# Optimization experiments

Measured on AMD Instinct MI355X. Metric: run time of the kernel, lower is better.

The kernel has to match this reference:

```python
import jax, jax.numpy as jnp
import numpy as np

FRAC_BITS = 16            # fixed-point fractional bits (MPC fixedpoint precision)
SCALE = float(1 << FRAC_BITS)

def fxp(v):
    """Emulate dup_with_precision: round value to the fixed-point grid with
    FRAC_BITS fractional bits. Straight-through (identity) gradient, matching
    the MPC backward pass which propagates gradients through truncation."""
    return v + jax.lax.stop_gradient(jnp.round(v * SCALE) / SCALE - v)


def setup_inputs() -> dict:
    key = jax.random.key(0)
    kx, kw = jax.random.split(key)
    in_dim, out_dim, batch = 4096, 4096, 2048
    x = jax.random.normal(kx, (batch, in_dim), dtype=jnp.float32)
    # Dense_Local init: w ~ N(0, 1/sqrt(in_dim+1)), b = zeros
    w = jax.random.normal(kw, (in_dim, out_dim), dtype=jnp.float32) / np.sqrt(in_dim + 1)
    b = jnp.zeros((out_dim,), dtype=jnp.float32)
    return {"x": x, "w": w, "b": b}


def reference(x, w, b):
    # quantize operands to the fixed-point grid (values live on the grid in MPC)
    xq = fxp(x)
    wq = fxp(w)
    # y = x @ w, then dup_with_precision(x.fixedpoint): truncate product back
    y = fxp(jnp.matmul(xq, wq))           # [batch, out_dim]
    # + bias
    y = y + fxp(b)
    # secure ReLU: s = drelu_local(y) (sign bit), y = relu(y, s) = y * s
    s = y >= 0
    y = jnp.where(s, y, jnp.zeros((), dtype=y.dtype))
    # final dup_with_precision(new_fixedpoint=x.fixedpoint)
    return fxp(y)
```

## Files before the change

### kernel.cpp

```cpp
#include <hip/hip_runtime.h>
#include <hip/hip_bf16.h>
#include <stdint.h>

#define M_DIM 2048
#define N_DIM 4096
#define K_DIM 4096

#define NT 64

typedef short short8 __attribute__((ext_vector_type(8)));
typedef float f32x4 __attribute__((ext_vector_type(4)));

typedef __attribute__((address_space(1))) unsigned int gu32;
typedef __attribute__((address_space(3))) unsigned int lu32;

__device__ static inline unsigned short f32_to_bf16(float f) {
  union { float f; unsigned int u; } v; v.f = f;
  unsigned int u = v.u;
  u += 0x7FFFu + ((u >> 16) & 1u);
  return (unsigned short)(u >> 16);
}

__global__ void cvt_x_kernel(const float* __restrict__ in, unsigned short* __restrict__ out) {
  size_t i = ((size_t)blockIdx.x * blockDim.x + threadIdx.x) * 8;
  f32x4 a = *(const f32x4*)(in + i);
  f32x4 b = *(const f32x4*)(in + i + 4);
  short8 o;
  o[0] = (short)f32_to_bf16(a[0]); o[1] = (short)f32_to_bf16(a[1]);
  o[2] = (short)f32_to_bf16(a[2]); o[3] = (short)f32_to_bf16(a[3]);
  o[4] = (short)f32_to_bf16(b[0]); o[5] = (short)f32_to_bf16(b[1]);
  o[6] = (short)f32_to_bf16(b[2]); o[7] = (short)f32_to_bf16(b[3]);
  *(short8*)(out + i) = o;
}

__global__ void transpose_cvt_w_kernel(const float* __restrict__ w, unsigned short* __restrict__ wt) {
  __shared__ unsigned short tile[64][64 + 8];
  int bn = blockIdx.x * 64;
  int bk = blockIdx.y * 64;
  int t = threadIdx.x;
  int c4 = (t & 15) * 4;
  int r0 = t >> 4;
#pragma unroll
  for (int p = 0; p < 4; ++p) {
    int r = r0 + p * 16;
    f32x4 v = *(const f32x4*)(w + (size_t)(bk + r) * N_DIM + bn + c4);
    tile[c4 + 0][r] = f32_to_bf16(v[0]);
    tile[c4 + 1][r] = f32_to_bf16(v[1]);
    tile[c4 + 2][r] = f32_to_bf16(v[2]);
    tile[c4 + 3][r] = f32_to_bf16(v[3]);
  }
  __syncthreads();
  int orow = t >> 2;
  int oc = (t & 3) * 16;
  short8 lo, hi;
#pragma unroll
  for (int j = 0; j < 8; ++j) {
    lo[j] = (short)tile[orow][oc + j];
    hi[j] = (short)tile[orow][oc + 8 + j];
  }
  unsigned short* op = wt + (size_t)(bn + orow) * K_DIM + bk + oc;
  *(short8*)(op) = lo;
  *(short8*)(op + 8) = hi;
}


__global__ __launch_bounds__(512) void gemm8_kernel(
    const unsigned short* __restrict__ A, const unsigned short* __restrict__ Bt,
    const float* __restrict__ bias, float* __restrict__ C) {
  __shared__ unsigned short sm16[3 * 24576];
  char* smem = (char*)&sm16[0];

  const int tid = threadIdx.x;
  const int lane = tid & 63;
  const int w = tid >> 6;
  const int wm = w >> 2, wn = w & 3;

  const int id = blockIdx.x;
  const int x = id & 7, j = id >> 3;
  const int by = ((x >> 2) << 3) + (j >> 2);
  const int bx = ((x & 3) << 2) + (j & 3);
  const int r0 = by * 128, c0 = bx * 256;

  const int l8 = lane >> 3, l7 = lane & 7;
  const int chunkE = ((l7 ^ (l8 & 7)) << 3);
  const unsigned short* Ag = A + (size_t)(r0 + w * 16 + l8) * K_DIM + chunkE;
  const unsigned short* Bg = Bt + (size_t)(c0 + w * 32 + l8) * K_DIM + chunkE;
  const int aL0 = w * 2048;
  const int bL0 = 16384 + w * 4096;

#define GL(gp, ldsoff) __builtin_amdgcn_global_load_lds((gu32*)(gp), (lu32*)(smem + (ldsoff)), 16, 0, 0)
#define STAGE_ALL(t, sb)                                               \
  do {                                                                 \
    GL(Ag + (size_t)(t) * 64, (sb) + aL0);                             \
    GL(Ag + (size_t)(t) * 64 + 8 * (size_t)K_DIM, (sb) + aL0 + 1024);  \
    GL(Bg + (size_t)(t) * 64, (sb) + bL0);                             \
    GL(Bg + (size_t)(t) * 64 + 8 * (size_t)K_DIM, (sb) + bL0 + 1024);  \
    GL(Bg + (size_t)(t) * 64 + 16 * (size_t)K_DIM, (sb) + bL0 + 2048); \
    GL(Bg + (size_t)(t) * 64 + 24 * (size_t)K_DIM, (sb) + bL0 + 3072); \
  } while (0)

  const int l15 = lane & 15, hi = lane >> 4;
  const int aR = (wm * 64 + l15) * 64;
  const int bR = 8192 + (wn * 64 + l15) * 64;
  const int slot0 = ((hi ^ l7) << 3);
  const int slot1 = (((4 + hi) ^ l7) << 3);

  f32x4 acc[4][4] = {};

  STAGE_ALL(0, 0);
  STAGE_ALL(1, 49152);

  int cs = 0;
  for (int t = 0; t < NT; ++t) {
    const int sE = cs * 24576;
    const int stB = (cs == 0 ? 2 : cs - 1) * 49152;
    const bool doStage = (t + 2) < NT;

    if (t < NT - 1) asm volatile("s_waitcnt vmcnt(6) lgkmcnt(0)" ::: "memory");
    else            asm volatile("s_waitcnt vmcnt(0) lgkmcnt(0)" ::: "memory");
    __builtin_amdgcn_sched_barrier(0);
    asm volatile("s_barrier" ::: "memory");

    short8 a0[4], b0[4], a1[4], b1[4];
#pragma unroll
    for (int m = 0; m < 4; ++m) a0[m] = *(const short8*)(sm16 + sE + aR + m * 1024 + slot0);
#pragma unroll
    for (int n = 0; n < 4; ++n) b0[n] = *(const short8*)(sm16 + sE + bR + n * 1024 + slot0);
    if (doStage) STAGE_ALL(t + 2, stB);
#pragma unroll
    for (int m = 0; m < 4; ++m) a1[m] = *(const short8*)(sm16 + sE + aR + m * 1024 + slot1);
#pragma unroll
    for (int n = 0; n < 4; ++n) b1[n] = *(const short8*)(sm16 + sE + bR + n * 1024 + slot1);

    __builtin_amdgcn_s_setprio(1);
#pragma unroll
    for (int m = 0; m < 4; ++m)
#pragma unroll
      for (int n = 0; n < 4; ++n)
        acc[m][n] = __builtin_amdgcn_mfma_f32_16x16x32_bf16(a0[m], b0[n], acc[m][n], 0, 0, 0);
#pragma unroll
    for (int m = 0; m < 4; ++m)
#pragma unroll
      for (int n = 0; n < 4; ++n)
        acc[m][n] = __builtin_amdgcn_mfma_f32_16x16x32_bf16(a1[m], b1[n], acc[m][n], 0, 0, 0);
    __builtin_amdgcn_s_setprio(0);

    cs = (cs == 2) ? 0 : cs + 1;
  }

  const float S = 65536.0f, IS = 1.0f / 65536.0f;
  const int lr = hi * 4;
#pragma unroll
  for (int n = 0; n < 4; ++n) {
    int gcol = c0 + wn * 64 + n * 16 + l15;
    float bq = rintf(bias[gcol] * S) * IS;
#pragma unroll
    for (int m = 0; m < 4; ++m) {
      int grow = r0 + wm * 64 + m * 16 + lr;
      float* outp = C + (size_t)grow * N_DIM + gcol;
#pragma unroll
      for (int r = 0; r < 4; ++r) {
        float t = rintf(acc[m][n][r] * S) * IS + bq;
        t = t > 0.0f ? t : 0.0f;
        outp[(size_t)r * N_DIM] = t;
      }
    }
  }
#undef GL
#undef STAGE_ALL
}

__global__ __launch_bounds__(256, 2) void gemm_fb_kernel(
    const float* __restrict__ Xf, const float* __restrict__ Wf,
    const float* __restrict__ bias, float* __restrict__ C) {
  __shared__ unsigned short As[128][64];
  __shared__ unsigned short Bs[128][64];
  int tid = threadIdx.x;
  int lane = tid & 63;
  int wid = tid >> 6;
  int wr = wid >> 1, wc = wid & 1;
  int r0 = blockIdx.y * 128;
  int c0 = blockIdx.x * 128;
  f32x4 acc[4][4] = {};
  for (int kt = 0; kt < K_DIM / 64; ++kt) {
    __syncthreads();
    int ar = tid >> 1;
    int ac = (tid & 1) * 32;
    const float* xp = Xf + (size_t)(r0 + ar) * K_DIM + kt * 64 + ac;
#pragma unroll
    for (int jj = 0; jj < 8; ++jj) {
      f32x4 v = *(const f32x4*)(xp + jj * 4);
      As[ar][ac + jj * 4 + 0] = f32_to_bf16(v[0]);
      As[ar][ac + jj * 4 + 1] = f32_to_bf16(v[1]);
      As[ar][ac + jj * 4 + 2] = f32_to_bf16(v[2]);
      As[ar][ac + jj * 4 + 3] = f32_to_bf16(v[3]);
    }
    int bk_ = tid >> 2;
    int bc = (tid & 3) * 32;
    const float* wp = Wf + (size_t)(kt * 64 + bk_) * N_DIM + c0 + bc;
#pragma unroll
    for (int jj = 0; jj < 8; ++jj) {
      f32x4 v = *(const f32x4*)(wp + jj * 4);
      Bs[bc + jj * 4 + 0][bk_] = f32_to_bf16(v[0]);
      Bs[bc + jj * 4 + 1][bk_] = f32_to_bf16(v[1]);
      Bs[bc + jj * 4 + 2][bk_] = f32_to_bf16(v[2]);
      Bs[bc + jj * 4 + 3][bk_] = f32_to_bf16(v[3]);
    }
    __syncthreads();
#pragma unroll
    for (int ks = 0; ks < 2; ++ks) {
      int co = ks * 32 + (lane >> 4) * 8;
      int rA = wr * 64 + (lane & 15);
      int rB = wc * 64 + (lane & 15);
      short8 a[4], b[4];
#pragma unroll
      for (int m = 0; m < 4; ++m) a[m] = *(const short8*)&As[rA + m * 16][co];
#pragma unroll
      for (int n = 0; n < 4; ++n) b[n] = *(const short8*)&Bs[rB + n * 16][co];
#pragma unroll
      for (int m = 0; m < 4; ++m)
#pragma unroll
        for (int n = 0; n < 4; ++n)
          acc[m][n] = __builtin_amdgcn_mfma_f32_16x16x32_bf16(a[m], b[n], acc[m][n], 0, 0, 0);
    }
  }
  const float S = 65536.0f, IS = 1.0f / 65536.0f;
  int lr = (lane >> 4) * 4;
  int lc = lane & 15;
#pragma unroll
  for (int n = 0; n < 4; ++n) {
    int gcol = c0 + wc * 64 + n * 16 + lc;
    float bq = rintf(bias[gcol] * S) * IS;
#pragma unroll
    for (int m = 0; m < 4; ++m) {
      int grow = r0 + wr * 64 + m * 16 + lr;
      float* outp = C + (size_t)grow * N_DIM + gcol;
#pragma unroll
      for (int r = 0; r < 4; ++r) {
        float t = rintf(acc[m][n][r] * S) * IS + bq;
        t = t > 0.0f ? t : 0.0f;
        outp[(size_t)r * N_DIM] = t;
      }
    }
  }
}

extern "C" void kernel_launch(void* const* d_in, const int* in_sizes, int n_in,
                              void* d_out, int out_size, void* d_ws, size_t ws_size,
                              hipStream_t stream) {
  const float* x = (const float*)d_in[0];
  const float* w = (const float*)d_in[1];
  const float* b = (const float*)d_in[2];
  float* out = (float*)d_out;

  size_t needA = (size_t)M_DIM * K_DIM * sizeof(unsigned short);
  size_t needB = (size_t)K_DIM * N_DIM * sizeof(unsigned short);

  if (ws_size >= needA + needB) {
    unsigned short* Abf = (unsigned short*)d_ws;
    unsigned short* Btbf = (unsigned short*)((char*)d_ws + needA);
    cvt_x_kernel<<<(M_DIM * (size_t)K_DIM / 8 + 255) / 256, 256, 0, stream>>>(x, Abf);
    transpose_cvt_w_kernel<<<dim3(N_DIM / 64, K_DIM / 64), 256, 0, stream>>>(w, Btbf);
    gemm8_kernel<<<256, 512, 0, stream>>>(Abf, Btbf, b, out);
  } else {
    gemm_fb_kernel<<<dim3(N_DIM / 128, M_DIM / 128), 256, 0, stream>>>(x, w, b, out);
  }
}
```

Before: 90.88 us.

## Unroll GEMM main loop by two with precomputed LDS stage pointers

```diff
diff --git a/kernel.cpp b/kernel.cpp
--- a/kernel.cpp
+++ b/kernel.cpp
@@ -67,8 +67,8 @@
 __global__ __launch_bounds__(512) void gemm8_kernel(
     const unsigned short* __restrict__ A, const unsigned short* __restrict__ Bt,
     const float* __restrict__ bias, float* __restrict__ C) {
-  __shared__ unsigned short sm16[3 * 24576];
-  char* smem = (char*)&sm16[0];
+  __shared__ unsigned short smA[3 * 24576];
+  char* smemc = (char*)&smA[0];
 
   const int tid = threadIdx.x;
   const int lane = tid & 63;
@@ -82,13 +82,13 @@
   const int r0 = by * 128, c0 = bx * 256;
 
   const int l8 = lane >> 3, l7 = lane & 7;
-  const int chunkE = ((l7 ^ (l8 & 7)) << 3);
+  const int chunkE = ((l7 ^ l8) << 3);
   const unsigned short* Ag = A + (size_t)(r0 + w * 16 + l8) * K_DIM + chunkE;
   const unsigned short* Bg = Bt + (size_t)(c0 + w * 32 + l8) * K_DIM + chunkE;
   const int aL0 = w * 2048;
   const int bL0 = 16384 + w * 4096;
 
-#define GL(gp, ldsoff) __builtin_amdgcn_global_load_lds((gu32*)(gp), (lu32*)(smem + (ldsoff)), 16, 0, 0)
+#define GL(gp, ldsoff) __builtin_amdgcn_global_load_lds((gu32*)(gp), (lu32*)(smemc + (ldsoff)), 16, 0, 0)
 #define STAGE_ALL(t, sb)                                               \
   do {                                                                 \
     GL(Ag + (size_t)(t) * 64, (sb) + aL0);                             \
@@ -104,6 +104,15 @@
   const int bR = 8192 + (wn * 64 + l15) * 64;
   const int slot0 = ((hi ^ l7) << 3);
   const int slot1 = (((4 + hi) ^ l7) << 3);
+  const unsigned short* pA[3][2];
+  const unsigned short* pB[3][2];
+#pragma unroll
+  for (int s = 0; s < 3; ++s) {
+    pA[s][0] = smA + s * 24576 + aR + slot0;
+    pA[s][1] = smA + s * 24576 + aR + slot1;
+    pB[s][0] = smA + s * 24576 + bR + slot0;
+    pB[s][1] = smA + s * 24576 + bR + slot1;
+  }
 
   f32x4 acc[4][4] = {};
 
@@ -111,41 +120,80 @@
   STAGE_ALL(1, 49152);
 
   int cs = 0;
-  for (int t = 0; t < NT; ++t) {
-    const int sE = cs * 24576;
-    const int stB = (cs == 0 ? 2 : cs - 1) * 49152;
-    const bool doStage = (t + 2) < NT;
-
-    if (t < NT - 1) asm volatile("s_waitcnt vmcnt(6) lgkmcnt(0)" ::: "memory");
-    else            asm volatile("s_waitcnt vmcnt(0) lgkmcnt(0)" ::: "memory");
-    __builtin_amdgcn_sched_barrier(0);
+  for (int jw = 0; jw < NT / 2; ++jw) {
+    const int t = jw * 2;
+    const int cs1 = (cs == 2) ? 0 : cs + 1;
+    const int cs2 = (cs1 == 2) ? 0 : cs1 + 1;
+    const bool doS = (t + 2) < NT;
+
+    const unsigned short* pAs0 = (cs == 0) ? pA[0][0] : (cs == 1) ? pA[1][0] : pA[2][0];
+    const unsigned short* pAs1 = (cs == 0) ? pA[0][1] : (cs == 1) ? pA[1][1] : pA[2][1];
+    const unsigned short* pBs0 = (cs == 0) ? pB[0][0] : (cs == 1) ? pB[1][0] : pB[2][0];
+    const unsigned short* pBs1 = (cs == 0) ? pB[0][1] : (cs == 1) ? pB[1][1] : pB[2][1];
+    const unsigned short* qAs0 = (cs1 == 0) ? pA[0][0] : (cs1 == 1) ? pA[1][0] : pA[2][0];
+    const unsigned short* qAs1 = (cs1 == 0) ? pA[0][1] : (cs1 == 1) ? pA[1][1] : pA[2][1];
+    const unsigned short* qBs0 = (cs1 == 0) ? pB[0][0] : (cs1 == 1) ? pB[1][0] : pB[2][0];
+    const unsigned short* qBs1 = (cs1 == 0) ? pB[0][1] : (cs1 == 1) ? pB[1][1] : pB[2][1];
+
+    asm volatile("s_waitcnt vmcnt(0) lgkmcnt(0)" ::: "memory");
     asm volatile("s_barrier" ::: "memory");
 
-    short8 a0[4], b0[4], a1[4], b1[4];
-#pragma unroll
-    for (int m = 0; m < 4; ++m) a0[m] = *(const short8*)(sm16 + sE + aR + m * 1024 + slot0);
-#pragma unroll
-    for (int n = 0; n < 4; ++n) b0[n] = *(const short8*)(sm16 + sE + bR + n * 1024 + slot0);
-    if (doStage) STAGE_ALL(t + 2, stB);
-#pragma unroll
-    for (int m = 0; m < 4; ++m) a1[m] = *(const short8*)(sm16 + sE + aR + m * 1024 + slot1);
-#pragma unroll
-    for (int n = 0; n < 4; ++n) b1[n] = *(const short8*)(sm16 + sE + bR + n * 1024 + slot1);
-
-    __builtin_amdgcn_s_setprio(1);
-#pragma unroll
-    for (int m = 0; m < 4; ++m)
-#pragma unroll
-      for (int n = 0; n < 4; ++n)
-        acc[m][n] = __builtin_amdgcn_mfma_f32_16x16x32_bf16(a0[m], b0[n], acc[m][n], 0, 0, 0);
-#pragma unroll
-    for (int m = 0; m < 4; ++m)
-#pragma unroll
-      for (int n = 0; n < 4; ++n)
-        acc[m][n] = __builtin_amdgcn_mfma_f32_16x16x32_bf16(a1[m], b1[n], acc[m][n], 0, 0, 0);
-    __builtin_amdgcn_s_setprio(0);
-
-    cs = (cs == 2) ? 0 : cs + 1;
+    {
+      short8 a0[4], b0[4], a1[4], b1[4];
+#pragma unroll
+      for (int m = 0; m < 4; ++m) a0[m] = *(const short8*)(pAs0 + m * 1024);
+#pragma unroll
+      for (int n = 0; n < 4; ++n) b0[n] = *(const short8*)(pBs0 + n * 1024);
+      if (doS) STAGE_ALL(t + 2, cs2 * 49152);
+#pragma unroll
+      for (int m = 0; m < 4; ++m) a1[m] = *(const short8*)(pAs1 + m * 1024);
+#pragma unroll
+      for (int n = 0; n < 4; ++n) b1[n] = *(const short8*)(pBs1 + n * 1024);
+
+      __builtin_amdgcn_s_setprio(1);
+#pragma unroll
+      for (int m = 0; m < 4; ++m)
+#pragma unroll
+        for (int n = 0; n < 4; ++n)
+          acc[m][n] = __builtin_amdgcn_mfma_f32_16x16x32_bf16(a0[m], b0[n], acc[m][n], 0, 0, 0);
+#pragma unroll
+      for (int m = 0; m < 4; ++m)
+#pragma unroll
+        for (int n = 0; n < 4; ++n)
+          acc[m][n] = __builtin_amdgcn_mfma_f32_16x16x32_bf16(a1[m], b1[n], acc[m][n], 0, 0, 0);
+      __builtin_amdgcn_s_setprio(0);
+    }
+
+    asm volatile("s_waitcnt lgkmcnt(0)" ::: "memory");
+    asm volatile("s_barrier" ::: "memory");
+
+    {
+      if (doS) STAGE_ALL(t + 3, cs * 49152);
+      short8 a0[4], b0[4], a1[4], b1[4];
+#pragma unroll
+      for (int m = 0; m < 4; ++m) a0[m] = *(const short8*)(qAs0 + m * 1024);
+#pragma unroll
+      for (int n = 0; n < 4; ++n) b0[n] = *(const short8*)(qBs0 + n * 1024);
+#pragma unroll
+      for (int m = 0; m < 4; ++m) a1[m] = *(const short8*)(qAs1 + m * 1024);
+#pragma unroll
+      for (int n = 0; n < 4; ++n) b1[n] = *(const short8*)(qBs1 + n * 1024);
+
+      __builtin_amdgcn_s_setprio(1);
+#pragma unroll
+      for (int m = 0; m < 4; ++m)
+#pragma unroll
+        for (int n = 0; n < 4; ++n)
+          acc[m][n] = __builtin_amdgcn_mfma_f32_16x16x32_bf16(a0[m], b0[n], acc[m][n], 0, 0, 0);
+#pragma unroll
+      for (int m = 0; m < 4; ++m)
+#pragma unroll
+        for (int n = 0; n < 4; ++n)
+          acc[m][n] = __builtin_amdgcn_mfma_f32_16x16x32_bf16(a1[m], b1[n], acc[m][n], 0, 0, 0);
+      __builtin_amdgcn_s_setprio(0);
+    }
+
+    cs = cs2;
   }
 
   const float S = 65536.0f, IS = 1.0f / 65536.0f;
```

After: 91.29 us. Within noise of the previous version (+0.4%).
